# Performance work log

Hardware: AMD Instinct MI355X
Metric: run time of the kernel (lower is better)

## Reference

```python
import jax, jax.numpy as jnp
import numpy as np

NUM_USERS = 100000
NUM_ITEMS = 200000
EMBED_DIM = 64
NUM_LAYERS = 3
NUM_EDGES = 1200000
BATCH = 4096


def setup_inputs() -> dict:
    key = jax.random.key(0)
    k0, k1, k2, k3 = jax.random.split(key, 4)
    n = NUM_USERS + NUM_ITEMS
    embedding_weight = 0.01 * jax.random.normal(k0, (n, EMBED_DIM), dtype=jnp.float32)
    edge_index = jax.random.randint(k1, (2, NUM_EDGES), 0, n, dtype=jnp.int64)
    user_indices = jax.random.randint(k2, (BATCH,), 0, NUM_USERS, dtype=jnp.int64)
    item_indices = jax.random.randint(k3, (BATCH,), 0, NUM_ITEMS, dtype=jnp.int64)
    return {
        "embedding_weight": embedding_weight,
        "edge_index": edge_index,
        "user_indices": user_indices,
        "item_indices": item_indices,
    }


def reference(embedding_weight, edge_index, user_indices, item_indices):
    n = NUM_USERS + NUM_ITEMS
    src, dst = edge_index[0], edge_index[1]
    # LightGCN propagation: gather by src, scatter-add by dst, per layer.
    cur = embedding_weight
    acc = embedding_weight  # running sum of layer outputs (layer 0 included)
    for _ in range(NUM_LAYERS):
        cur = jax.ops.segment_sum(cur[src], dst, num_segments=n)
        acc = acc + cur
    final = acc / jnp.asarray(NUM_LAYERS + 1, dtype=acc.dtype)
    user_emb = final[user_indices]                       # [B, D] (users occupy rows [0, NUM_USERS))
    item_emb = final[NUM_USERS + item_indices]           # [B, D]
    return jnp.sum(user_emb * item_emb, axis=1, keepdims=True)  # [B, 1]
```

## Files before the change

### kernel.cpp

```cpp
#include <hip/hip_runtime.h>

#define NUM_USERS 100000
#define NUM_ITEMS 200000
#define NNODES    300000
#define EDIM      64
#define NEDGES    1200000
#define BATCH     4096
#define CHUNK     1024
#define NCHUNKS   ((NNODES + CHUNK - 1) / CHUNK)
#define NBLKN     ((NNODES + 255) / 256)
#define EBLK4     ((NEDGES / 4 + 255) / 256)

static inline size_t align256(size_t x) { return (x + 255) & ~(size_t)255; }

__device__ __forceinline__ void f4add(float4& a, const float4& b) {
    a.x += b.x; a.y += b.y; a.z += b.z; a.w += b.w;
}


__global__ void mark_sampled_k(const int* __restrict__ users, const int* __restrict__ items,
                               unsigned char* __restrict__ mS) {
    int t = (int)(blockIdx.x * blockDim.x + threadIdx.x);
    if (t >= 2 * BATCH) return;
    int node = (t < BATCH) ? users[t] : (NUM_USERS + items[t - BATCH]);
    mS[node] = 1;
}

__global__ void markA_k(const int* __restrict__ src, const int* __restrict__ dst,
                        const unsigned char* __restrict__ mS, unsigned char* __restrict__ mA) {
    int base = (int)(blockIdx.x * blockDim.x + threadIdx.x) * 4;
    if (base >= NEDGES) return;
    int4 d4 = *(const int4*)(dst + base);
    unsigned char a0 = mS[d4.x], a1 = mS[d4.y], a2 = mS[d4.z], a3 = mS[d4.w];
    if (a0 | a1 | a2 | a3) {
        int4 s4 = *(const int4*)(src + base);
        if (a0) mA[s4.x] = 1;
        if (a1) mA[s4.y] = 1;
        if (a2) mA[s4.z] = 1;
        if (a3) mA[s4.w] = 1;
    }
}

__global__ void markB_k(const int* __restrict__ src, const int* __restrict__ dst,
                        const unsigned char* __restrict__ mS, const unsigned char* __restrict__ mA,
                        unsigned char* __restrict__ mB) {
    int base = (int)(blockIdx.x * blockDim.x + threadIdx.x) * 4;
    if (base >= NEDGES) return;
    int4 d4 = *(const int4*)(dst + base);
    unsigned char a0 = mS[d4.x] | mA[d4.x];
    unsigned char a1 = mS[d4.y] | mA[d4.y];
    unsigned char a2 = mS[d4.z] | mA[d4.z];
    unsigned char a3 = mS[d4.w] | mA[d4.w];
    if (a0 | a1 | a2 | a3) {
        int4 s4 = *(const int4*)(src + base);
        if (a0) mB[s4.x] = 1;
        if (a1) mB[s4.y] = 1;
        if (a2) mB[s4.z] = 1;
        if (a3) mB[s4.w] = 1;
    }
}

__global__ void combine_k(const unsigned char* __restrict__ mS, const unsigned char* __restrict__ mA,
                          const unsigned char* __restrict__ mB, unsigned char* __restrict__ need) {
    int i = (int)(blockIdx.x * blockDim.x + threadIdx.x);
    if (i >= NNODES) return;
    unsigned char s = mS[i], a = mA[i], b = mB[i];
    need[i] = (unsigned char)(((s | a | b) ? 1 : 0) | ((s | a) ? 2 : 0));
}

__global__ void hist_epos_gated_k(const int* __restrict__ dst, int* __restrict__ counts,
                                  int* __restrict__ epos, const unsigned char* __restrict__ need) {
    int base = (int)(blockIdx.x * blockDim.x + threadIdx.x) * 4;
    if (base >= NEDGES) return;
    int4 d4 = *(const int4*)(dst + base);
    bool g0 = need[d4.x] & 1, g1 = need[d4.y] & 1, g2 = need[d4.z] & 1, g3 = need[d4.w] & 1;
    if (g0) epos[base + 0] = atomicAdd(&counts[d4.x], 1);
    if (g1) epos[base + 1] = atomicAdd(&counts[d4.y], 1);
    if (g2) epos[base + 2] = atomicAdd(&counts[d4.z], 1);
    if (g3) epos[base + 3] = atomicAdd(&counts[d4.w], 1);
}

__global__ void scan_chunk_k(const int* __restrict__ counts, int* __restrict__ row_ptr,
                             int* __restrict__ chunk_tot) {
    __shared__ int sm[256];
    int t = threadIdx.x;
    int base = (int)blockIdx.x * CHUNK + t * 4;
    int v0 = (base + 0 < NNODES) ? counts[base + 0] : 0;
    int v1 = (base + 1 < NNODES) ? counts[base + 1] : 0;
    int v2 = (base + 2 < NNODES) ? counts[base + 2] : 0;
    int v3 = (base + 3 < NNODES) ? counts[base + 3] : 0;
    int ts = v0 + v1 + v2 + v3;
    sm[t] = ts;
    __syncthreads();
    for (int off = 1; off < 256; off <<= 1) {
        int x = (t >= off) ? sm[t - off] : 0;
        __syncthreads();
        sm[t] += x;
        __syncthreads();
    }
    int run = sm[t] - ts;
    if (t == 255) chunk_tot[blockIdx.x] = sm[255];
    if (base + 0 < NNODES) row_ptr[base + 0] = run; run += v0;
    if (base + 1 < NNODES) row_ptr[base + 1] = run; run += v1;
    if (base + 2 < NNODES) row_ptr[base + 2] = run; run += v2;
    if (base + 3 < NNODES) row_ptr[base + 3] = run;
}

__global__ void scan_tops_k(int* __restrict__ chunk_tot, int* __restrict__ row_ptr) {
    int lane = threadIdx.x & 63;
    int carry = 0;
    for (int base = 0; base < NCHUNKS; base += 64) {
        int idx = base + lane;
        int v = (idx < NCHUNKS) ? chunk_tot[idx] : 0;
        int x = v;
        #pragma unroll
        for (int off = 1; off < 64; off <<= 1) {
            int t = __shfl_up(x, off, 64);
            if (lane >= off) x += t;
        }
        if (idx < NCHUNKS) chunk_tot[idx] = carry + x - v;
        carry += __shfl(x, 63, 64);
    }
    if (lane == 0) row_ptr[NNODES] = carry;
}

__global__ void add_off_k(int* __restrict__ row_ptr, const int* __restrict__ chunk_tot) {
    int i = (int)(blockIdx.x * blockDim.x + threadIdx.x);
    if (i < NNODES) row_ptr[i] += chunk_tot[i / CHUNK];
}

__global__ void fill_epos_k(const int* __restrict__ src, const int* __restrict__ dst,
                            const int* __restrict__ row_ptr, const int* __restrict__ epos,
                            int* __restrict__ ssrc, const unsigned char* __restrict__ need) {
    int base = (int)(blockIdx.x * blockDim.x + threadIdx.x) * 4;
    if (base >= NEDGES) return;
    int4 d4 = *(const int4*)(dst + base);
    bool g0 = need[d4.x] & 1, g1 = need[d4.y] & 1, g2 = need[d4.z] & 1, g3 = need[d4.w] & 1;
    if (!(g0 | g1 | g2 | g3)) return;
    int4 s4 = *(const int4*)(src + base);
    int4 p4 = *(const int4*)(epos + base);
    if (g0) ssrc[row_ptr[d4.x] + p4.x] = s4.x;
    if (g1) ssrc[row_ptr[d4.y] + p4.y] = s4.y;
    if (g2) ssrc[row_ptr[d4.z] + p4.z] = s4.z;
    if (g3) ssrc[row_ptr[d4.w] + p4.w] = s4.w;
}


__global__ void count_wl_k(const unsigned char* __restrict__ mS, const unsigned char* __restrict__ mA,
                           const unsigned char* __restrict__ mB, int* __restrict__ cnt1,
                           int* __restrict__ cnt2) {
    __shared__ int w1[4], w2[4];
    int i = (int)(blockIdx.x * blockDim.x + threadIdx.x);
    int lane = threadIdx.x & 63, wv = threadIdx.x >> 6;
    unsigned char s = 0, a = 0, b = 0;
    if (i < NNODES) { s = mS[i]; a = mA[i]; b = mB[i]; }
    bool p1 = (i < NNODES) && (s | a | b);
    bool p2 = (i < NNODES) && (s | a);
    unsigned long long b1 = __ballot(p1), b2 = __ballot(p2);
    if (lane == 0) { w1[wv] = __popcll(b1); w2[wv] = __popcll(b2); }
    __syncthreads();
    if (threadIdx.x == 0) {
        cnt1[blockIdx.x] = w1[0] + w1[1] + w1[2] + w1[3];
        cnt2[blockIdx.x] = w2[0] + w2[1] + w2[2] + w2[3];
    }
}

__global__ void scan_blocks_k(int* __restrict__ cnt1, int* __restrict__ cnt2, int* __restrict__ wl_n) {
    int lane = threadIdx.x & 63;
    int carry1 = 0, carry2 = 0;
    for (int base = 0; base < NBLKN; base += 64) {
        int idx = base + lane;
        int v1 = (idx < NBLKN) ? cnt1[idx] : 0;
        int v2 = (idx < NBLKN) ? cnt2[idx] : 0;
        int x1 = v1, x2 = v2;
        #pragma unroll
        for (int off = 1; off < 64; off <<= 1) {
            int t1 = __shfl_up(x1, off, 64);
            int t2 = __shfl_up(x2, off, 64);
            if (lane >= off) { x1 += t1; x2 += t2; }
        }
        if (idx < NBLKN) { cnt1[idx] = carry1 + x1 - v1; cnt2[idx] = carry2 + x2 - v2; }
        carry1 += __shfl(x1, 63, 64);
        carry2 += __shfl(x2, 63, 64);
    }
    if (lane == 0) { wl_n[0] = carry1; wl_n[1] = carry2; }
}

__global__ void emit_wl_k(const unsigned char* __restrict__ mS, const unsigned char* __restrict__ mA,
                          const unsigned char* __restrict__ mB, const int* __restrict__ cnt1,
                          const int* __restrict__ cnt2, int* __restrict__ wl1, int* __restrict__ wl2) {
    __shared__ int w1[4], w2[4];
    int i = (int)(blockIdx.x * blockDim.x + threadIdx.x);
    int lane = threadIdx.x & 63, wv = threadIdx.x >> 6;
    unsigned char s = 0, a = 0, b = 0;
    if (i < NNODES) { s = mS[i]; a = mA[i]; b = mB[i]; }
    bool p1 = (i < NNODES) && (s | a | b);
    bool p2 = (i < NNODES) && (s | a);
    unsigned long long b1 = __ballot(p1), b2 = __ballot(p2);
    if (lane == 0) { w1[wv] = __popcll(b1); w2[wv] = __popcll(b2); }
    __syncthreads();
    int off1 = 0, off2 = 0;
    for (int k = 0; k < wv; ++k) { off1 += w1[k]; off2 += w2[k]; }
    unsigned long long lt = (1ULL << lane) - 1;
    if (p1) wl1[cnt1[blockIdx.x] + off1 + __popcll(b1 & lt)] = i;
    if (p2) wl2[cnt2[blockIdx.x] + off2 + __popcll(b2 & lt)] = i;
}


#define PROP_BLOCKS 2048

__global__ __launch_bounds__(256) void prop_f4_k(
        const float* __restrict__ cur, float* __restrict__ nxt,
        const int* __restrict__ row_ptr, const int* __restrict__ ssrc,
        const int* __restrict__ wl, const int* __restrict__ n_ptr) {
    int lane = threadIdx.x & 63;
    int sub = lane >> 4, d16 = lane & 15;
    int gw = (int)((blockIdx.x * blockDim.x + threadIdx.x) >> 6);
    int nw = (int)((gridDim.x * blockDim.x) >> 6);
    int n = *n_ptr;
    int nhalf = (n + 1) >> 1;
    const float4* cur4 = (const float4*)cur;
    if (gw >= nhalf) return;

    int i = gw;
    int nodeA = wl[i];
    int nodeB = (i + nhalf < n) ? wl[i + nhalf] : -1;
    int a0 = row_ptr[nodeA], a1 = row_ptr[nodeA + 1];
    int b0 = 0, b1 = 0;
    if (nodeB >= 0) { b0 = row_ptr[nodeB]; b1 = row_ptr[nodeB + 1]; }
    int iaA = (a0 + sub     < a1) ? ssrc[a0 + sub]     : -1;
    int ibA = (a0 + 4 + sub < a1) ? ssrc[a0 + 4 + sub] : -1;
    int iaB = (b0 + sub     < b1) ? ssrc[b0 + sub]     : -1;
    int ibB = (b0 + 4 + sub < b1) ? ssrc[b0 + 4 + sub] : -1;

    while (true) {
        int j = i + nw;
        bool have_next = (j < nhalf);
        int nnA = 0, nnB = -1, na0 = 0, na1 = 0, nb0 = 0, nb1 = 0;
        int niaA = -1, nibA = -1, niaB = -1, nibB = -1;
        if (have_next) {
            nnA = wl[j];
            nnB = (j + nhalf < n) ? wl[j + nhalf] : -1;
            na0 = row_ptr[nnA]; na1 = row_ptr[nnA + 1];
            if (nnB >= 0) { nb0 = row_ptr[nnB]; nb1 = row_ptr[nnB + 1]; }
            niaA = (na0 + sub     < na1) ? ssrc[na0 + sub]     : -1;
            nibA = (na0 + 4 + sub < na1) ? ssrc[na0 + 4 + sub] : -1;
            niaB = (nb0 + sub     < nb1) ? ssrc[nb0 + sub]     : -1;
            nibB = (nb0 + 4 + sub < nb1) ? ssrc[nb0 + 4 + sub] : -1;
        }
        float4 aA0 = {0.f,0.f,0.f,0.f}, aA1 = {0.f,0.f,0.f,0.f};
        float4 aB0 = {0.f,0.f,0.f,0.f}, aB1 = {0.f,0.f,0.f,0.f};
        if (iaA >= 0) f4add(aA0, cur4[(size_t)iaA * 16 + d16]);
        if (ibA >= 0) f4add(aA1, cur4[(size_t)ibA * 16 + d16]);
        if (iaB >= 0) f4add(aB0, cur4[(size_t)iaB * 16 + d16]);
        if (ibB >= 0) f4add(aB1, cur4[(size_t)ibB * 16 + d16]);
        for (int e = a0 + 8; e < a1; e += 8) {
            int p = e + sub, q = e + 4 + sub;
            if (p < a1) f4add(aA0, cur4[(size_t)ssrc[p] * 16 + d16]);
            if (q < a1) f4add(aA1, cur4[(size_t)ssrc[q] * 16 + d16]);
        }
        for (int e = b0 + 8; e < b1; e += 8) {
            int p = e + sub, q = e + 4 + sub;
            if (p < b1) f4add(aB0, cur4[(size_t)ssrc[p] * 16 + d16]);
            if (q < b1) f4add(aB1, cur4[(size_t)ssrc[q] * 16 + d16]);
        }
        f4add(aA0, aA1);
        aA0.x += __shfl_xor(aA0.x, 16, 64); aA0.x += __shfl_xor(aA0.x, 32, 64);
        aA0.y += __shfl_xor(aA0.y, 16, 64); aA0.y += __shfl_xor(aA0.y, 32, 64);
        aA0.z += __shfl_xor(aA0.z, 16, 64); aA0.z += __shfl_xor(aA0.z, 32, 64);
        aA0.w += __shfl_xor(aA0.w, 16, 64); aA0.w += __shfl_xor(aA0.w, 32, 64);
        if (sub == 0) ((float4*)nxt)[(size_t)nodeA * 16 + d16] = aA0;
        if (nodeB >= 0) {
            f4add(aB0, aB1);
            aB0.x += __shfl_xor(aB0.x, 16, 64); aB0.x += __shfl_xor(aB0.x, 32, 64);
            aB0.y += __shfl_xor(aB0.y, 16, 64); aB0.y += __shfl_xor(aB0.y, 32, 64);
            aB0.z += __shfl_xor(aB0.z, 16, 64); aB0.z += __shfl_xor(aB0.z, 32, 64);
            aB0.w += __shfl_xor(aB0.w, 16, 64); aB0.w += __shfl_xor(aB0.w, 32, 64);
            if (sub == 0) ((float4*)nxt)[(size_t)nodeB * 16 + d16] = aB0;
        }
        if (!have_next) break;
        i = j;
        nodeA = nnA; nodeB = nnB;
        a0 = na0; a1 = na1; b0 = nb0; b1 = nb1;
        iaA = niaA; ibA = nibA; iaB = niaB; ibB = nibB;
    }
}


__device__ __forceinline__ float4 gather_row_sum(const float4* __restrict__ b4,
                                                 const int* __restrict__ ssrc,
                                                 int s0, int s1, int sub, int d16) {
    float4 acc0 = {0.f, 0.f, 0.f, 0.f}, acc1 = {0.f, 0.f, 0.f, 0.f};
    for (int e = s0; e < s1; e += 8) {
        int p = e + sub, q = e + 4 + sub;
        if (p < s1) f4add(acc0, b4[(size_t)ssrc[p] * 16 + d16]);
        if (q < s1) f4add(acc1, b4[(size_t)ssrc[q] * 16 + d16]);
    }
    f4add(acc0, acc1);
    return acc0;
}

__global__ __launch_bounds__(256) void final_dot_k(
        const float* __restrict__ emb, const float* __restrict__ bufA,
        const float* __restrict__ bufB, const int* __restrict__ users,
        const int* __restrict__ items, const int* __restrict__ row_ptr,
        const int* __restrict__ ssrc, float* __restrict__ out) {
    int t = (int)(blockIdx.x * blockDim.x + threadIdx.x);
    int b = t >> 6;
    if (b >= BATCH) return;
    int lane = threadIdx.x & 63, sub = lane >> 4, d16 = lane & 15;
    int nu = users[b], ni = NUM_USERS + items[b];
    int u0 = row_ptr[nu], u1 = row_ptr[nu + 1];
    int i0 = row_ptr[ni], i1 = row_ptr[ni + 1];
    const float4* b4 = (const float4*)bufB;
    float4 au = gather_row_sum(b4, ssrc, u0, u1, sub, d16);
    float4 ai = gather_row_sum(b4, ssrc, i0, i1, sub, d16);
    au.x += __shfl_xor(au.x, 16, 64); au.x += __shfl_xor(au.x, 32, 64);
    au.y += __shfl_xor(au.y, 16, 64); au.y += __shfl_xor(au.y, 32, 64);
    au.z += __shfl_xor(au.z, 16, 64); au.z += __shfl_xor(au.z, 32, 64);
    au.w += __shfl_xor(au.w, 16, 64); au.w += __shfl_xor(au.w, 32, 64);
    ai.x += __shfl_xor(ai.x, 16, 64); ai.x += __shfl_xor(ai.x, 32, 64);
    ai.y += __shfl_xor(ai.y, 16, 64); ai.y += __shfl_xor(ai.y, 32, 64);
    ai.z += __shfl_xor(ai.z, 16, 64); ai.z += __shfl_xor(ai.z, 32, 64);
    ai.w += __shfl_xor(ai.w, 16, 64); ai.w += __shfl_xor(ai.w, 32, 64);
    if (sub == 0) {
        size_t ru = (size_t)nu * 16 + d16, ri = (size_t)ni * 16 + d16;
        float4 eu = ((const float4*)emb)[ru], pu = ((const float4*)bufA)[ru], qu = ((const float4*)bufB)[ru];
        float4 ei = ((const float4*)emb)[ri], pi = ((const float4*)bufA)[ri], qi = ((const float4*)bufB)[ri];
        float fx = (eu.x + pu.x + qu.x + au.x) * (ei.x + pi.x + qi.x + ai.x);
        float fy = (eu.y + pu.y + qu.y + au.y) * (ei.y + pi.y + qi.y + ai.y);
        float fz = (eu.z + pu.z + qu.z + au.z) * (ei.z + pi.z + qi.z + ai.z);
        float fw = (eu.w + pu.w + qu.w + au.w) * (ei.w + pi.w + qi.w + ai.w);
        float p = fx + fy + fz + fw;
        p += __shfl_xor(p, 1, 64); p += __shfl_xor(p, 2, 64);
        p += __shfl_xor(p, 4, 64); p += __shfl_xor(p, 8, 64);
        if (d16 == 0) out[b] = p * (1.0f / 16.0f);
    }
}


__global__ void acc_batch_k(const float* __restrict__ cur, const int* __restrict__ users,
                            const int* __restrict__ items, float* __restrict__ accs, int first) {
    int t = (int)(blockIdx.x * blockDim.x + threadIdx.x);
    int row = t >> 6, lane = t & 63;
    if (row >= 2 * BATCH) return;
    int node = (row < BATCH) ? users[row] : (NUM_USERS + items[row - BATCH]);
    float v = cur[(size_t)node * EDIM + lane];
    size_t o = (size_t)row * EDIM + lane;
    if (first) accs[o] = v;
    else       accs[o] += v;
}

__global__ void scatter_add_k(const float* __restrict__ cur, float* __restrict__ nxt,
                              const int* __restrict__ src, const int* __restrict__ dst) {
    int w = (int)((blockIdx.x * blockDim.x + threadIdx.x) >> 6);
    int lane = threadIdx.x & 63;
    if (w >= NEDGES) return;
    float v = cur[(size_t)src[w] * EDIM + lane];
    atomicAdd(&nxt[(size_t)dst[w] * EDIM + lane], v);
}

__global__ void dot_out_k(const float* __restrict__ accs, float* __restrict__ out) {
    int t = (int)(blockIdx.x * blockDim.x + threadIdx.x);
    int b = t >> 6, lane = t & 63;
    if (b >= BATCH) return;
    float p = accs[(size_t)b * EDIM + lane] * accs[(size_t)(BATCH + b) * EDIM + lane];
    #pragma unroll
    for (int off = 32; off; off >>= 1) p += __shfl_down(p, off, 64);
    if (lane == 0) out[b] = p * (1.0f / 16.0f);
}

extern "C" void kernel_launch(void* const* d_in, const int* in_sizes, int n_in,
                              void* d_out, int out_size, void* d_ws, size_t ws_size,
                              hipStream_t stream) {
    const float* emb   = (const float*)d_in[0];
    const int*   edge  = (const int*)d_in[1];
    const int*   src   = edge;
    const int*   dst   = edge + NEDGES;
    const int*   users = (const int*)d_in[2];
    const int*   items = (const int*)d_in[3];
    float*       out   = (float*)d_out;

    const size_t bufBytes = (size_t)NNODES * EDIM * sizeof(float);

    size_t off = 0;
    float* bufA = (float*)((char*)d_ws + off); off = align256(off + bufBytes);
    float* bufB = (float*)((char*)d_ws + off); off = align256(off + bufBytes);
    float* accs = (float*)((char*)d_ws + off); off = align256(off + (size_t)2 * BATCH * EDIM * sizeof(float));
    int* row_ptr = (int*)((char*)d_ws + off); off = align256(off + (size_t)(NNODES + 1) * sizeof(int));
    int* ssrc    = (int*)((char*)d_ws + off); off = align256(off + (size_t)NEDGES * sizeof(int));
    int* epos    = (int*)((char*)d_ws + off); off = align256(off + (size_t)NEDGES * sizeof(int));
    int* wl1     = (int*)((char*)d_ws + off); off = align256(off + (size_t)NNODES * sizeof(int));
    int* wl2     = (int*)((char*)d_ws + off); off = align256(off + (size_t)NNODES * sizeof(int));
    int* cnt1    = (int*)((char*)d_ws + off); off = align256(off + (size_t)NBLKN * sizeof(int));
    int* cnt2    = (int*)((char*)d_ws + off); off = align256(off + (size_t)NBLKN * sizeof(int));
    int* wl_n    = (int*)((char*)d_ws + off); off = align256(off + 2 * sizeof(int));
    int* chunk_tot = (int*)((char*)d_ws + off); off = align256(off + (size_t)NCHUNKS * sizeof(int));
    unsigned char* need = (unsigned char*)((char*)d_ws + off); off = align256(off + (size_t)NNODES);
    const size_t zeroBase = off;
    int* counts    = (int*)((char*)d_ws + off); off += (size_t)NNODES * sizeof(int);
    unsigned char* mS = (unsigned char*)((char*)d_ws + off); off += (size_t)NNODES;
    unsigned char* mA = (unsigned char*)((char*)d_ws + off); off += (size_t)NNODES;
    unsigned char* mB = (unsigned char*)((char*)d_ws + off); off += (size_t)NNODES;
    const size_t zeroBytes = off - zeroBase;
    const size_t needed = align256(off);

    const dim3 blk(256);
    const int nodeBlocks = NBLKN;
    const int sampBlocks = (2 * BATCH * 64 + 255) / 256;
    const int dotBlocks  = (BATCH * 64 + 255) / 256;

    if (ws_size >= needed) {
        hipMemsetAsync((char*)d_ws + zeroBase, 0, zeroBytes, stream);
        mark_sampled_k<<<(2 * BATCH + 255) / 256, blk, 0, stream>>>(users, items, mS);
        markA_k<<<EBLK4, blk, 0, stream>>>(src, dst, mS, mA);
        markB_k<<<EBLK4, blk, 0, stream>>>(src, dst, mS, mA, mB);
        combine_k<<<nodeBlocks, blk, 0, stream>>>(mS, mA, mB, need);
        hist_epos_gated_k<<<EBLK4, blk, 0, stream>>>(dst, counts, epos, need);
        scan_chunk_k<<<NCHUNKS, blk, 0, stream>>>(counts, row_ptr, chunk_tot);
        scan_tops_k<<<1, 64, 0, stream>>>(chunk_tot, row_ptr);
        add_off_k<<<nodeBlocks, blk, 0, stream>>>(row_ptr, chunk_tot);
        fill_epos_k<<<EBLK4, blk, 0, stream>>>(src, dst, row_ptr, epos, ssrc, need);
        count_wl_k<<<nodeBlocks, blk, 0, stream>>>(mS, mA, mB, cnt1, cnt2);
        scan_blocks_k<<<1, 64, 0, stream>>>(cnt1, cnt2, wl_n);
        emit_wl_k<<<nodeBlocks, blk, 0, stream>>>(mS, mA, mB, cnt1, cnt2, wl1, wl2);

        prop_f4_k<<<PROP_BLOCKS, blk, 0, stream>>>(emb,  bufA, row_ptr, ssrc, wl1, wl_n);
        prop_f4_k<<<PROP_BLOCKS, blk, 0, stream>>>(bufA, bufB, row_ptr, ssrc, wl2, wl_n + 1);
        final_dot_k<<<dotBlocks, blk, 0, stream>>>(emb, bufA, bufB, users, items, row_ptr, ssrc, out);
    } else {
        const int scatterBlocks = (NEDGES + 3) / 4;
        acc_batch_k<<<sampBlocks, blk, 0, stream>>>(emb, users, items, accs, 1);
        const float* cur = emb;
        float* bufs[2] = {bufA, bufB};
        for (int l = 0; l < 3; ++l) {
            float* nxt = bufs[l & 1];
            hipMemsetAsync(nxt, 0, bufBytes, stream);
            scatter_add_k<<<scatterBlocks, blk, 0, stream>>>(cur, nxt, src, dst);
            acc_batch_k<<<sampBlocks, blk, 0, stream>>>(nxt, users, items, accs, 0);
            cur = nxt;
        }
        dot_out_k<<<dotBlocks, blk, 0, stream>>>(accs, out);
    }
}
```

Measured before the change: 145.0 us.

## Store intermediate layer embeddings as bf16 and trim the layer-1 worklist

The propagation kernels now write layer-1 and layer-2 embeddings as packed bf16 and read them back with unpacking, which halves the bytes moved by the random row gathers in the second propagation pass and in the final dot. The layer-1 worklist predicate changes from s|a|b to s|b, so fewer nodes are computed in the first pass. The cost is bf16 rounding error in the propagated sums. The reduced worklist could also drop nodes that later stages still read if the mask semantics do not line up.

```diff
diff --git a/kernel.cpp b/kernel.cpp
--- a/kernel.cpp
+++ b/kernel.cpp
@@ -15,6 +15,25 @@
 
 __device__ __forceinline__ void f4add(float4& a, const float4& b) {
     a.x += b.x; a.y += b.y; a.z += b.z; a.w += b.w;
+}
+
+__device__ __forceinline__ unsigned bf16_1(float x) {
+    unsigned u = __float_as_uint(x);
+    return (u + 0x7FFFu + ((u >> 16) & 1u)) >> 16;
+}
+__device__ __forceinline__ uint2 pack_bf16x4(float4 v) {
+    uint2 r;
+    r.x = bf16_1(v.x) | (bf16_1(v.y) << 16);
+    r.y = bf16_1(v.z) | (bf16_1(v.w) << 16);
+    return r;
+}
+__device__ __forceinline__ float4 unpack_bf16x4(uint2 p) {
+    float4 v;
+    v.x = __uint_as_float(p.x << 16);
+    v.y = __uint_as_float(p.x & 0xFFFF0000u);
+    v.z = __uint_as_float(p.y << 16);
+    v.w = __uint_as_float(p.y & 0xFFFF0000u);
+    return v;
 }
 
 
@@ -154,7 +173,7 @@
     int lane = threadIdx.x & 63, wv = threadIdx.x >> 6;
     unsigned char s = 0, a = 0, b = 0;
     if (i < NNODES) { s = mS[i]; a = mA[i]; b = mB[i]; }
-    bool p1 = (i < NNODES) && (s | a | b);
+    bool p1 = (i < NNODES) && (s | b);
     bool p2 = (i < NNODES) && (s | a);
     unsigned long long b1 = __ballot(p1), b2 = __ballot(p2);
     if (lane == 0) { w1[wv] = __popcll(b1); w2[wv] = __popcll(b2); }
@@ -194,7 +213,7 @@
     int lane = threadIdx.x & 63, wv = threadIdx.x >> 6;
     unsigned char s = 0, a = 0, b = 0;
     if (i < NNODES) { s = mS[i]; a = mA[i]; b = mB[i]; }
-    bool p1 = (i < NNODES) && (s | a | b);
+    bool p1 = (i < NNODES) && (s | b);
     bool p2 = (i < NNODES) && (s | a);
     unsigned long long b1 = __ballot(p1), b2 = __ballot(p2);
     if (lane == 0) { w1[wv] = __popcll(b1); w2[wv] = __popcll(b2); }
@@ -209,8 +228,17 @@
 
 #define PROP_BLOCKS 2048
 
-__global__ __launch_bounds__(256) void prop_f4_k(
-        const float* __restrict__ cur, float* __restrict__ nxt,
+template<bool SRC_BF16>
+__device__ __forceinline__ float4 ld_row(const float4* __restrict__ c4,
+                                         const uint2* __restrict__ cb, int idx, int d16) {
+    if constexpr (SRC_BF16) return unpack_bf16x4(cb[(size_t)idx * 16 + d16]);
+    else                    return c4[(size_t)idx * 16 + d16];
+}
+
+template<bool SRC_BF16>
+__global__ __launch_bounds__(256) void prop_dual_k(
+        const float4* __restrict__ cur4, const uint2* __restrict__ curb,
+        uint2* __restrict__ nxtb,
         const int* __restrict__ row_ptr, const int* __restrict__ ssrc,
         const int* __restrict__ wl, const int* __restrict__ n_ptr) {
     int lane = threadIdx.x & 63;
@@ -219,7 +247,6 @@
     int nw = (int)((gridDim.x * blockDim.x) >> 6);
     int n = *n_ptr;
     int nhalf = (n + 1) >> 1;
-    const float4* cur4 = (const float4*)cur;
     if (gw >= nhalf) return;
 
     int i = gw;
@@ -250,33 +277,33 @@
         }
         float4 aA0 = {0.f,0.f,0.f,0.f}, aA1 = {0.f,0.f,0.f,0.f};
         float4 aB0 = {0.f,0.f,0.f,0.f}, aB1 = {0.f,0.f,0.f,0.f};
-        if (iaA >= 0) f4add(aA0, cur4[(size_t)iaA * 16 + d16]);
-        if (ibA >= 0) f4add(aA1, cur4[(size_t)ibA * 16 + d16]);
-        if (iaB >= 0) f4add(aB0, cur4[(size_t)iaB * 16 + d16]);
-        if (ibB >= 0) f4add(aB1, cur4[(size_t)ibB * 16 + d16]);
+        if (iaA >= 0) f4add(aA0, ld_row<SRC_BF16>(cur4, curb, iaA, d16));
+        if (ibA >= 0) f4add(aA1, ld_row<SRC_BF16>(cur4, curb, ibA, d16));
+        if (iaB >= 0) f4add(aB0, ld_row<SRC_BF16>(cur4, curb, iaB, d16));
+        if (ibB >= 0) f4add(aB1, ld_row<SRC_BF16>(cur4, curb, ibB, d16));
         for (int e = a0 + 8; e < a1; e += 8) {
             int p = e + sub, q = e + 4 + sub;
-            if (p < a1) f4add(aA0, cur4[(size_t)ssrc[p] * 16 + d16]);
-            if (q < a1) f4add(aA1, cur4[(size_t)ssrc[q] * 16 + d16]);
+            if (p < a1) f4add(aA0, ld_row<SRC_BF16>(cur4, curb, ssrc[p], d16));
+            if (q < a1) f4add(aA1, ld_row<SRC_BF16>(cur4, curb, ssrc[q], d16));
         }
         for (int e = b0 + 8; e < b1; e += 8) {
             int p = e + sub, q = e + 4 + sub;
-            if (p < b1) f4add(aB0, cur4[(size_t)ssrc[p] * 16 + d16]);
-            if (q < b1) f4add(aB1, cur4[(size_t)ssrc[q] * 16 + d16]);
+            if (p < b1) f4add(aB0, ld_row<SRC_BF16>(cur4, curb, ssrc[p], d16));
+            if (q < b1) f4add(aB1, ld_row<SRC_BF16>(cur4, curb, ssrc[q], d16));
         }
         f4add(aA0, aA1);
         aA0.x += __shfl_xor(aA0.x, 16, 64); aA0.x += __shfl_xor(aA0.x, 32, 64);
         aA0.y += __shfl_xor(aA0.y, 16, 64); aA0.y += __shfl_xor(aA0.y, 32, 64);
         aA0.z += __shfl_xor(aA0.z, 16, 64); aA0.z += __shfl_xor(aA0.z, 32, 64);
         aA0.w += __shfl_xor(aA0.w, 16, 64); aA0.w += __shfl_xor(aA0.w, 32, 64);
-        if (sub == 0) ((float4*)nxt)[(size_t)nodeA * 16 + d16] = aA0;
+        if (sub == 0) nxtb[(size_t)nodeA * 16 + d16] = pack_bf16x4(aA0);
         if (nodeB >= 0) {
             f4add(aB0, aB1);
             aB0.x += __shfl_xor(aB0.x, 16, 64); aB0.x += __shfl_xor(aB0.x, 32, 64);
             aB0.y += __shfl_xor(aB0.y, 16, 64); aB0.y += __shfl_xor(aB0.y, 32, 64);
             aB0.z += __shfl_xor(aB0.z, 16, 64); aB0.z += __shfl_xor(aB0.z, 32, 64);
             aB0.w += __shfl_xor(aB0.w, 16, 64); aB0.w += __shfl_xor(aB0.w, 32, 64);
-            if (sub == 0) ((float4*)nxt)[(size_t)nodeB * 16 + d16] = aB0;
+            if (sub == 0) nxtb[(size_t)nodeB * 16 + d16] = pack_bf16x4(aB0);
         }
         if (!have_next) break;
         i = j;
@@ -287,22 +314,22 @@
 }
 
 
-__device__ __forceinline__ float4 gather_row_sum(const float4* __restrict__ b4,
-                                                 const int* __restrict__ ssrc,
-                                                 int s0, int s1, int sub, int d16) {
+__device__ __forceinline__ float4 gather_row_sum_b(const uint2* __restrict__ bb,
+                                                   const int* __restrict__ ssrc,
+                                                   int s0, int s1, int sub, int d16) {
     float4 acc0 = {0.f, 0.f, 0.f, 0.f}, acc1 = {0.f, 0.f, 0.f, 0.f};
     for (int e = s0; e < s1; e += 8) {
         int p = e + sub, q = e + 4 + sub;
-        if (p < s1) f4add(acc0, b4[(size_t)ssrc[p] * 16 + d16]);
-        if (q < s1) f4add(acc1, b4[(size_t)ssrc[q] * 16 + d16]);
+        if (p < s1) f4add(acc0, unpack_bf16x4(bb[(size_t)ssrc[p] * 16 + d16]));
+        if (q < s1) f4add(acc1, unpack_bf16x4(bb[(size_t)ssrc[q] * 16 + d16]));
     }
     f4add(acc0, acc1);
     return acc0;
 }
 
 __global__ __launch_bounds__(256) void final_dot_k(
-        const float* __restrict__ emb, const float* __restrict__ bufA,
-        const float* __restrict__ bufB, const int* __restrict__ users,
+        const float* __restrict__ emb, const uint2* __restrict__ bufA,
+        const uint2* __restrict__ bufB, const int* __restrict__ users,
         const int* __restrict__ items, const int* __restrict__ row_ptr,
         const int* __restrict__ ssrc, float* __restrict__ out) {
     int t = (int)(blockIdx.x * blockDim.x + threadIdx.x);
@@ -312,9 +339,8 @@
     int nu = users[b], ni = NUM_USERS + items[b];
     int u0 = row_ptr[nu], u1 = row_ptr[nu + 1];
     int i0 = row_ptr[ni], i1 = row_ptr[ni + 1];
-    const float4* b4 = (const float4*)bufB;
-    float4 au = gather_row_sum(b4, ssrc, u0, u1, sub, d16);
-    float4 ai = gather_row_sum(b4, ssrc, i0, i1, sub, d16);
+    float4 au = gather_row_sum_b(bufB, ssrc, u0, u1, sub, d16);
+    float4 ai = gather_row_sum_b(bufB, ssrc, i0, i1, sub, d16);
     au.x += __shfl_xor(au.x, 16, 64); au.x += __shfl_xor(au.x, 32, 64);
     au.y += __shfl_xor(au.y, 16, 64); au.y += __shfl_xor(au.y, 32, 64);
     au.z += __shfl_xor(au.z, 16, 64); au.z += __shfl_xor(au.z, 32, 64);
@@ -325,8 +351,10 @@
     ai.w += __shfl_xor(ai.w, 16, 64); ai.w += __shfl_xor(ai.w, 32, 64);
     if (sub == 0) {
         size_t ru = (size_t)nu * 16 + d16, ri = (size_t)ni * 16 + d16;
-        float4 eu = ((const float4*)emb)[ru], pu = ((const float4*)bufA)[ru], qu = ((const float4*)bufB)[ru];
-        float4 ei = ((const float4*)emb)[ri], pi = ((const float4*)bufA)[ri], qi = ((const float4*)bufB)[ri];
+        float4 eu = ((const float4*)emb)[ru];
+        float4 ei = ((const float4*)emb)[ri];
+        float4 pu = unpack_bf16x4(bufA[ru]), qu = unpack_bf16x4(bufB[ru]);
+        float4 pi = unpack_bf16x4(bufA[ri]), qi = unpack_bf16x4(bufB[ri]);
         float fx = (eu.x + pu.x + qu.x + au.x) * (ei.x + pi.x + qi.x + ai.x);
         float fy = (eu.y + pu.y + qu.y + au.y) * (ei.y + pi.y + qi.y + ai.y);
         float fz = (eu.z + pu.z + qu.z + au.z) * (ei.z + pi.z + qi.z + ai.z);
@@ -411,6 +439,9 @@
     const int dotBlocks  = (BATCH * 64 + 255) / 256;
 
     if (ws_size >= needed) {
+        uint2* bufAb = (uint2*)bufA;
+        uint2* bufBb = (uint2*)bufB;
+
         hipMemsetAsync((char*)d_ws + zeroBase, 0, zeroBytes, stream);
         mark_sampled_k<<<(2 * BATCH + 255) / 256, blk, 0, stream>>>(users, items, mS);
         markA_k<<<EBLK4, blk, 0, stream>>>(src, dst, mS, mA);
@@ -425,9 +456,11 @@
         scan_blocks_k<<<1, 64, 0, stream>>>(cnt1, cnt2, wl_n);
         emit_wl_k<<<nodeBlocks, blk, 0, stream>>>(mS, mA, mB, cnt1, cnt2, wl1, wl2);
 
-        prop_f4_k<<<PROP_BLOCKS, blk, 0, stream>>>(emb,  bufA, row_ptr, ssrc, wl1, wl_n);
-        prop_f4_k<<<PROP_BLOCKS, blk, 0, stream>>>(bufA, bufB, row_ptr, ssrc, wl2, wl_n + 1);
-        final_dot_k<<<dotBlocks, blk, 0, stream>>>(emb, bufA, bufB, users, items, row_ptr, ssrc, out);
+        prop_dual_k<false><<<PROP_BLOCKS, blk, 0, stream>>>(
+            (const float4*)emb, nullptr, bufAb, row_ptr, ssrc, wl1, wl_n);
+        prop_dual_k<true><<<PROP_BLOCKS, blk, 0, stream>>>(
+            nullptr, (const uint2*)bufAb, bufBb, row_ptr, ssrc, wl2, wl_n + 1);
+        final_dot_k<<<dotBlocks, blk, 0, stream>>>(emb, bufAb, bufBb, users, items, row_ptr, ssrc, out);
     } else {
         const int scatterBlocks = (NEDGES + 3) / 4;
         acc_batch_k<<<sampBlocks, blk, 0, stream>>>(emb, users, items, accs, 1);
```

New measurement: 142.5 us. No clear change (-1.7%).
